# Kernel tuning notes

Measured on AMD Instinct MI355X. Metric: run time of the kernel, lower is better.

Reference implementation:

```python
import jax, jax.numpy as jnp
import numpy as np

N = 50000
NEG_SLOPE = 0.2  # PyG GATConv default leaky_relu slope


def _gat_layer(x, src, dst, W, a_s, a_d, b):
    # x: [N, Fin]; W: [Fin, H*C]; a_s, a_d: [H, C]; b: [C]
    H, C = a_s.shape
    xp = (x @ W).reshape(N, H, C)                      # projected node features per head
    alpha_s = jnp.einsum('nhc,hc->nh', xp, a_s)        # [N, H]
    alpha_d = jnp.einsum('nhc,hc->nh', xp, a_d)        # [N, H]
    e = jax.nn.leaky_relu(alpha_s[src] + alpha_d[dst], NEG_SLOPE)  # [E, H]
    # segment softmax over incoming edges of each dst node
    m = jax.ops.segment_max(e, dst, num_segments=N)
    m = jnp.where(jnp.isfinite(m), m, 0.0)
    p = jnp.exp(e - jax.lax.stop_gradient(m)[dst])
    denom = jax.ops.segment_sum(p, dst, num_segments=N)
    alpha = p / denom[dst]                             # [E, H]
    # scatter-aggregate messages
    out = jax.ops.segment_sum(alpha[:, :, None] * xp[src], dst, num_segments=N)  # [N, H, C]
    return out.mean(axis=1) + b                        # concat=False -> mean over heads


def setup_inputs() -> dict:
    key = jax.random.key(0)
    ks = jax.random.split(key, 16)
    IN, HID, OUT, H = 128, 64, 40, 4
    E = 800000
    x = jax.random.normal(ks[0], (N, IN), dtype=jnp.float32)
    edge_index = jax.random.randint(ks[1], (2, E), 0, N, dtype=jnp.int64)

    def mk(kw, ka, fin, fout):
        s = 1.0 / np.sqrt(fin)
        W = jax.random.normal(kw, (fin, H * fout), dtype=jnp.float32) * s
        a_s = jax.random.normal(ka, (H, fout), dtype=jnp.float32) * 0.1
        a_d = jax.random.normal(jax.random.fold_in(ka, 1), (H, fout), dtype=jnp.float32) * 0.1
        b = jnp.zeros((fout,), dtype=jnp.float32)
        return W, a_s, a_d, b

    W1, as1, ad1, b1 = mk(ks[2], ks[3], IN, HID)
    W2, as2, ad2, b2 = mk(ks[4], ks[5], HID, HID)
    W3, as3, ad3, b3 = mk(ks[6], ks[7], HID, OUT)
    return dict(x=x, edge_index=edge_index,
                W1=W1, as1=as1, ad1=ad1, b1=b1,
                W2=W2, as2=as2, ad2=ad2, b2=b2,
                W3=W3, as3=as3, ad3=ad3, b3=b3)


def reference(x, edge_index, W1, as1, ad1, b1, W2, as2, ad2, b2, W3, as3, ad3, b3):
    # PyG GATConv adds self-loops by default
    loop = jnp.arange(N, dtype=edge_index.dtype)
    src = jnp.concatenate([edge_index[0], loop])
    dst = jnp.concatenate([edge_index[1], loop])
    h = jax.nn.relu(_gat_layer(x, src, dst, W1, as1, ad1, b1))   # dropout is identity in eval
    h = jax.nn.relu(_gat_layer(h, src, dst, W2, as2, ad2, b2))
    h = jax.nn.relu(_gat_layer(h, src, dst, W3, as3, ad3, b3))
    return jax.nn.log_softmax(h, axis=-1)
```

## Files before the change

### kernel.cpp

```cpp
#include <hip/hip_runtime.h>
#include <math.h>

#define NNODES 50000
#define NEG_SLOPE 0.2f

typedef unsigned short ushort8v __attribute__((ext_vector_type(8)));
typedef unsigned short ushort4v __attribute__((ext_vector_type(4)));
typedef short short8v __attribute__((ext_vector_type(8)));
typedef float f32x4 __attribute__((ext_vector_type(4)));
typedef float f32x2 __attribute__((ext_vector_type(2)));

__device__ __forceinline__ unsigned short f2bf(float f){
    unsigned u = __float_as_uint(f);
    u += 0x7fff + ((u >> 16) & 1);
    return (unsigned short)(u >> 16);
}

__device__ __forceinline__ void emit_wa(const float* __restrict__ W, const float* __restrict__ a_s,
                                        const float* __restrict__ a_d, unsigned short* __restrict__ Wt,
                                        int Kin, int C, int id){
    const int n = id / Kin, k = id - n * Kin;
    float v = 0.f;
    if(n < 8){
        const int hh = n & 3;
        const float* av = (n < 4) ? a_s : a_d;
        for(int c = 0; c < C; c++) v += W[(size_t)k * (4 * C) + hh * C + c] * av[hh * C + c];
    }
    Wt[id] = f2bf(v);
}

__device__ __forceinline__ void emit_wc(const float* __restrict__ W, unsigned short* __restrict__ Wt,
                                        int Kin, int C, int id){
    const int c = id / (4 * Kin);
    const int hk = id - c * (4 * Kin);
    const int h = hk / Kin, k = hk - h * Kin;
    const float v = (c < C) ? W[(size_t)k * (4 * C) + h * C + c] * 0.25f : 0.f;
    Wt[id] = f2bf(v);
}

__global__ void initprep_kernel(const unsigned long long* __restrict__ e, int* __restrict__ flag,
                                int* __restrict__ deg, int N,
                                const float* __restrict__ x, unsigned short* __restrict__ xbf, int X4,
                                const float* __restrict__ W1, const float* __restrict__ as1, const float* __restrict__ ad1,
                                const float* __restrict__ W2, const float* __restrict__ as2, const float* __restrict__ ad2,
                                const float* __restrict__ W3, const float* __restrict__ as3, const float* __restrict__ ad3,
                                unsigned short* __restrict__ Wa1, unsigned short* __restrict__ Wa2,
                                unsigned short* __restrict__ Wa3, unsigned short* __restrict__ Wc1,
                                unsigned short* __restrict__ Wc2, unsigned short* __restrict__ Wc3){
    if(blockIdx.x == 0 && threadIdx.x < 64){
        const unsigned long long v = e[threadIdx.x];
        const unsigned long long mask = __ballot(v >= (1ULL << 32));
        if(threadIdx.x == 0) *flag = (mask == 0ULL) ? 1 : 0;
    }
    int id = blockIdx.x * blockDim.x + threadIdx.x;
    if(id < N) deg[id] = 0;
    if(id < X4){
        const float4 v = *(const float4*)&x[(size_t)id * 4];
        ushort4v o;
        o[0] = f2bf(v.x); o[1] = f2bf(v.y); o[2] = f2bf(v.z); o[3] = f2bf(v.w);
        *(ushort4v*)&xbf[(size_t)id * 4] = o;
        return;
    }
    id -= X4;
    if(id < 16 * 128){ emit_wa(W1, as1, ad1, Wa1, 128, 64, id); return; }
    id -= 16 * 128;
    if(id < 16 * 64){ emit_wa(W2, as2, ad2, Wa2, 64, 64, id); return; }
    id -= 16 * 64;
    if(id < 16 * 64){ emit_wa(W3, as3, ad3, Wa3, 64, 40, id); return; }
    id -= 16 * 64;
    if(id < 64 * 512){ emit_wc(W1, Wc1, 128, 64, id); return; }
    id -= 64 * 512;
    if(id < 64 * 256){ emit_wc(W2, Wc2, 64, 64, id); return; }
    id -= 64 * 256;
    if(id < 48 * 256){ emit_wc(W3, Wc3, 64, 40, id); }
}

__global__ void hist_kernel(const void* __restrict__ e, const int* __restrict__ flag,
                            int* __restrict__ deg, int E){
    const int i = blockIdx.x * blockDim.x + threadIdx.x;
    if(i < E){
        const int d = (*flag) ? (int)((const long long*)e)[E + i] : ((const int*)e)[E + i];
        atomicAdd(&deg[d], 1);
    }
}

__global__ __launch_bounds__(512) void scan1_kernel(const int* __restrict__ deg,
                                                    int* __restrict__ excl,
                                                    int* __restrict__ bsum, int n){
    __shared__ int sh[512];
    const int t = threadIdx.x;
    const int gid = blockIdx.x * 512 + t;
    const int v = (gid < n) ? deg[gid] : 0;
    sh[t] = v;
    __syncthreads();
    for(int off = 1; off < 512; off <<= 1){
        const int add = (t >= off) ? sh[t - off] : 0;
        __syncthreads();
        sh[t] += add;
        __syncthreads();
    }
    if(gid < n) excl[gid] = sh[t] - v;
    if(t == 511) bsum[blockIdx.x] = sh[511];
}

__global__ __launch_bounds__(128) void scan2_kernel(int* __restrict__ bsum, int nb){
    __shared__ int sh[128];
    const int t = threadIdx.x;
    const int v = (t < nb) ? bsum[t] : 0;
    sh[t] = v;
    __syncthreads();
    for(int off = 1; off < 128; off <<= 1){
        const int add = (t >= off) ? sh[t - off] : 0;
        __syncthreads();
        sh[t] += add;
        __syncthreads();
    }
    if(t < nb) bsum[t] = sh[t] - v;
}

__global__ void scan3_kernel(const int* __restrict__ excl, const int* __restrict__ bsum,
                             int* __restrict__ row_ptr, int* __restrict__ cursor,
                             int n, int E){
    const int gid = blockIdx.x * blockDim.x + threadIdx.x;
    if(gid < n){
        const int r = excl[gid] + bsum[gid >> 9];
        row_ptr[gid] = r;
        cursor[gid] = r;
    }
    if(gid == 0) row_ptr[n] = E;
}

__global__ void scatter_kernel(const void* __restrict__ e, const int* __restrict__ flag,
                               int* __restrict__ cursor, int* __restrict__ col, int E){
    const int i = blockIdx.x * blockDim.x + threadIdx.x;
    if(i < E){
        int s, d;
        if(*flag){ s = (int)((const long long*)e)[i]; d = (int)((const long long*)e)[E + i]; }
        else     { s = ((const int*)e)[i];            d = ((const int*)e)[E + i]; }
        const int pos = atomicAdd(&cursor[d], 1);
        col[pos] = s;
    }
}

template<int K>
__global__ __launch_bounds__(256) void agemm_kernel(const unsigned short* __restrict__ A,
                                                    const unsigned short* __restrict__ Wa,
                                                    float* __restrict__ ea, float* __restrict__ ed,
                                                    int M){
    const int lane = threadIdx.x & 63;
    const int wave = threadIdx.x >> 6;
    const int quad = lane >> 4;
    const int l16 = lane & 15;
    const int bm = blockIdx.x * 64;
    const int m = min(bm + wave * 16 + l16, M - 1);
    f32x4 acc = {0,0,0,0};
    #pragma unroll
    for(int k0 = 0; k0 < K; k0 += 32){
        const short8v a = *(const short8v*)&A[(size_t)m * K + k0 + quad * 8];
        const short8v b = *(const short8v*)&Wa[(size_t)l16 * K + k0 + quad * 8];
        acc = __builtin_amdgcn_mfma_f32_16x16x32_bf16(a, b, acc, 0, 0, 0);
    }
    if(l16 < 8){
        const int h = l16 & 3;
        float* dst = (l16 < 4) ? ea : ed;
        const int rbase = bm + wave * 16 + quad * 4;
        #pragma unroll
        for(int r = 0; r < 4; r++){
            const int row = rbase + r;
            if(row < M){
                const float v = acc[r];
                *(f32x2*)&dst[(size_t)row * 8 + 2 * h] = (f32x2){__expf(v), __expf(NEG_SLOPE * v)};
            }
        }
    }
}

template<int K>
__global__ __launch_bounds__(256) void gather_kernel(const unsigned short* __restrict__ X,
                                                     const int* __restrict__ row_ptr,
                                                     const int* __restrict__ col,
                                                     const float* __restrict__ ea,
                                                     const float* __restrict__ ed,
                                                     unsigned short* __restrict__ g){
    constexpr int CPL = K / 16;
    constexpr int PAIRS = CPL / 2;
    const int lane = threadIdx.x & 63;
    const int wave = threadIdx.x >> 6;
    const int n = blockIdx.x * 4 + wave;
    const int slot = lane >> 4;
    const int pos = lane & 15;
    const int rs = row_ptr[n], re = row_ptr[n + 1];
    const int T = re - rs + 1;
    const float4 edA = *(const float4*)&ed[(size_t)n * 8];
    const float4 edB = *(const float4*)&ed[(size_t)n * 8 + 4];

    f32x2 acc[4][PAIRS];
    #pragma unroll
    for(int h = 0; h < 4; h++)
        #pragma unroll
        for(int p = 0; p < PAIRS; p++) acc[h][p] = (f32x2){0.f, 0.f};
    float dnm[4] = {0.f, 0.f, 0.f, 0.f};

    auto body = [&](int e){
        const int s = (e < re) ? col[e] : n;
        const float4 eaA = *(const float4*)&ea[(size_t)s * 8];
        const float4 eaB = *(const float4*)&ea[(size_t)s * 8 + 4];
        const float w0 = fmaxf(eaA.x * edA.x, eaA.y * edA.y);
        const float w1 = fmaxf(eaA.z * edA.z, eaA.w * edA.w);
        const float w2 = fmaxf(eaB.x * edB.x, eaB.y * edB.y);
        const float w3 = fmaxf(eaB.z * edB.z, eaB.w * edB.w);
        dnm[0] += w0; dnm[1] += w1; dnm[2] += w2; dnm[3] += w3;
        unsigned u[PAIRS];
        if constexpr(PAIRS == 2){
            const uint2 t2 = *(const uint2*)&X[(size_t)s * K + pos * CPL];
            u[0] = t2.x; u[1] = t2.y;
        } else {
            const uint4 t4 = *(const uint4*)&X[(size_t)s * K + pos * CPL];
            u[0] = t4.x; u[1] = t4.y; u[2] = t4.z; u[3] = t4.w;
        }
        #pragma unroll
        for(int p = 0; p < PAIRS; p++){
            const f32x2 v = {__uint_as_float(u[p] << 16), __uint_as_float(u[p] & 0xffff0000u)};
            acc[0][p] += (f32x2){w0, w0} * v;
            acc[1][p] += (f32x2){w1, w1} * v;
            acc[2][p] += (f32x2){w2, w2} * v;
            acc[3][p] += (f32x2){w3, w3} * v;
        }
    };

    int k = 0;
    for(; k + 8 <= T; k += 8){ body(rs + k + slot); body(rs + k + 4 + slot); }
    for(; k + 4 <= T; k += 4){ body(rs + k + slot); }
    if(k < T && slot < T - k){ body(rs + k + slot); }

    #pragma unroll
    for(int msk = 16; msk < 64; msk <<= 1){
        #pragma unroll
        for(int h = 0; h < 4; h++){
            #pragma unroll
            for(int p = 0; p < PAIRS; p++){
                acc[h][p][0] += __shfl_xor(acc[h][p][0], msk);
                acc[h][p][1] += __shfl_xor(acc[h][p][1], msk);
            }
            dnm[h] += __shfl_xor(dnm[h], msk);
        }
    }
    if(lane < 16){
        #pragma unroll
        for(int h = 0; h < 4; h++){
            const float sc = 1.f / dnm[h];
            if constexpr(PAIRS == 2){
                ushort4v o;
                o[0] = f2bf(acc[h][0][0] * sc); o[1] = f2bf(acc[h][0][1] * sc);
                o[2] = f2bf(acc[h][1][0] * sc); o[3] = f2bf(acc[h][1][1] * sc);
                *(ushort4v*)&g[(size_t)n * (4 * K) + h * K + pos * CPL] = o;
            } else {
                ushort8v o;
                #pragma unroll
                for(int p = 0; p < 4; p++){
                    o[2*p]   = f2bf(acc[h][p][0] * sc);
                    o[2*p+1] = f2bf(acc[h][p][1] * sc);
                }
                *(ushort8v*)&g[(size_t)n * (4 * K) + h * K + pos * CPL] = o;
            }
        }
    }
}

template<int KC, int NC, bool FINAL, bool ALPHA>
__global__ __launch_bounds__(256) void pgemm_kernel(const unsigned short* __restrict__ A,
                                                    const unsigned short* __restrict__ Bt,
                                                    const float* __restrict__ bias,
                                                    void* __restrict__ outv,
                                                    const unsigned short* __restrict__ Wa,
                                                    float* __restrict__ ea,
                                                    float* __restrict__ ed,
                                                    int M){
    constexpr int NT = (NC + 15) / 16;
    __shared__ unsigned short lh[ALPHA ? 4 : 1][16][72];
    const int lane = threadIdx.x & 63;
    const int wave = threadIdx.x >> 6;
    const int quad = lane >> 4;
    const int l16 = lane & 15;
    const int bm = blockIdx.x * 64;
    const int m = min(bm + wave * 16 + l16, M - 1);
    const size_t arow = (size_t)m * KC;

    f32x4 acc[NT];
    #pragma unroll
    for(int t = 0; t < NT; t++) acc[t] = (f32x4){0,0,0,0};

    for(int k0 = 0; k0 < KC; k0 += 32){
        const short8v a = *(const short8v*)&A[arow + k0 + quad * 8];
        #pragma unroll
        for(int t = 0; t < NT; t++){
            const short8v b = *(const short8v*)&Bt[(size_t)(t * 16 + l16) * KC + k0 + quad * 8];
            acc[t] = __builtin_amdgcn_mfma_f32_16x16x32_bf16(a, b, acc[t], 0, 0, 0);
        }
    }
    const int rbase = bm + wave * 16 + quad * 4;
    if(!FINAL){
        unsigned short* out = (unsigned short*)outv;
        #pragma unroll
        for(int t = 0; t < NT; t++){
            const int c = t * 16 + l16;
            #pragma unroll
            for(int r = 0; r < 4; r++){
                const unsigned short hb = f2bf(fmaxf(acc[t][r] + bias[c], 0.f));
                const int row = rbase + r;
                if(row < M) out[(size_t)row * NC + c] = hb;
                if constexpr(ALPHA) lh[wave][quad * 4 + r][c] = hb;
            }
        }
        if constexpr(ALPHA){
            f32x4 a4 = {0, 0, 0, 0};
            #pragma unroll
            for(int k0 = 0; k0 < 64; k0 += 32){
                const short8v a = *(const short8v*)&lh[wave][l16][k0 + quad * 8];
                const short8v b = *(const short8v*)&Wa[(size_t)l16 * 64 + k0 + quad * 8];
                a4 = __builtin_amdgcn_mfma_f32_16x16x32_bf16(a, b, a4, 0, 0, 0);
            }
            if(l16 < 8){
                const int h = l16 & 3;
                float* dst = (l16 < 4) ? ea : ed;
                #pragma unroll
                for(int r = 0; r < 4; r++){
                    const int row = rbase + r;
                    if(row < M){
                        const float v = a4[r];
                        *(f32x2*)&dst[(size_t)row * 8 + 2 * h] = (f32x2){__expf(v), __expf(NEG_SLOPE * v)};
                    }
                }
            }
        }
    } else {
        float* out = (float*)outv;
        float o[NT][4];
        #pragma unroll
        for(int t = 0; t < NT; t++){
            const int c = t * 16 + l16;
            const bool valid = c < 40;
            const float bc = valid ? bias[c] : 0.f;
            #pragma unroll
            for(int r = 0; r < 4; r++)
                o[t][r] = valid ? fmaxf(acc[t][r] + bc, 0.f) : -INFINITY;
        }
        #pragma unroll
        for(int r = 0; r < 4; r++){
            float mx = o[0][r];
            #pragma unroll
            for(int t = 1; t < NT; t++) mx = fmaxf(mx, o[t][r]);
            #pragma unroll
            for(int off = 1; off < 16; off <<= 1) mx = fmaxf(mx, __shfl_xor(mx, off));
            float se = 0.f;
            #pragma unroll
            for(int t = 0; t < NT; t++) se += (o[t][r] > -INFINITY) ? __expf(o[t][r] - mx) : 0.f;
            #pragma unroll
            for(int off = 1; off < 16; off <<= 1) se += __shfl_xor(se, off);
            const float lz = mx + logf(se);
            const int row = rbase + r;
            if(row < M){
                #pragma unroll
                for(int t = 0; t < NT; t++){
                    const int c = t * 16 + l16;
                    if(c < 40) out[(size_t)row * 40 + c] = o[t][r] - lz;
                }
            }
        }
    }
}

extern "C" void kernel_launch(void* const* d_in, const int* in_sizes, int n_in,
                              void* d_out, int out_size, void* d_ws, size_t ws_size,
                              hipStream_t stream){
    const int N = NNODES;
    const int E = in_sizes[1] / 2;

    const float* x   = (const float*)d_in[0];
    const float* W1  = (const float*)d_in[2];
    const float* as1 = (const float*)d_in[3];
    const float* ad1 = (const float*)d_in[4];
    const float* b1  = (const float*)d_in[5];
    const float* W2  = (const float*)d_in[6];
    const float* as2 = (const float*)d_in[7];
    const float* ad2 = (const float*)d_in[8];
    const float* b2  = (const float*)d_in[9];
    const float* W3  = (const float*)d_in[10];
    const float* as3 = (const float*)d_in[11];
    const float* ad3 = (const float*)d_in[12];
    const float* b3  = (const float*)d_in[13];

    char* ws = (char*)d_ws;
    size_t off = 0;
    auto alloc = [&](size_t bytes) -> void* {
        void* p = ws + off;
        off = (off + bytes + 255) & ~(size_t)255;
        return p;
    };
    int*   flag    = (int*)  alloc(4);
    int*   row_ptr = (int*)  alloc((size_t)(N + 1) * 4);
    int*   colv    = (int*)  alloc((size_t)E * 4);
    int*   cursor  = (int*)  alloc((size_t)N * 4);
    int*   deg     = (int*)  alloc((size_t)N * 4);
    int*   excl    = (int*)  alloc((size_t)N * 4);
    int*   bsum    = (int*)  alloc(128 * 4);
    unsigned short* xbf = (unsigned short*)alloc((size_t)N * 128 * 2);
    unsigned short* Wa1 = (unsigned short*)alloc(16 * 128 * 2);
    unsigned short* Wa2 = (unsigned short*)alloc(16 * 64 * 2);
    unsigned short* Wa3 = (unsigned short*)alloc(16 * 64 * 2);
    unsigned short* Wc1 = (unsigned short*)alloc((size_t)64 * 512 * 2);
    unsigned short* Wc2 = (unsigned short*)alloc((size_t)64 * 256 * 2);
    unsigned short* Wc3 = (unsigned short*)alloc((size_t)48 * 256 * 2);
    float* eav     = (float*)alloc((size_t)N * 8 * 4);
    float* edv     = (float*)alloc((size_t)N * 8 * 4);
    unsigned short* g   = (unsigned short*)alloc((size_t)N * 512 * 2);
    unsigned short* h1  = (unsigned short*)alloc((size_t)N * 64 * 2);
    unsigned short* h2  = (unsigned short*)alloc((size_t)N * 64 * 2);
    (void)ws_size;

    const void* eraw = d_in[1];

    const int X4 = N * 128 / 4;
    const int prepTotal = X4 + 16*128 + 16*64 + 16*64 + 64*512 + 64*256 + 48*256;
    initprep_kernel<<<(prepTotal + 255) / 256, 256, 0, stream>>>(
        (const unsigned long long*)eraw, flag, deg, N, x, xbf, X4,
        W1, as1, ad1, W2, as2, ad2, W3, as3, ad3,
        Wa1, Wa2, Wa3, Wc1, Wc2, Wc3);

    hist_kernel<<<(E + 255) / 256, 256, 0, stream>>>(eraw, flag, deg, E);
    const int nbScan = (N + 511) / 512;
    scan1_kernel<<<nbScan, 512, 0, stream>>>(deg, excl, bsum, N);
    scan2_kernel<<<1, 128, 0, stream>>>(bsum, nbScan);
    scan3_kernel<<<(N + 255) / 256, 256, 0, stream>>>(excl, bsum, row_ptr, cursor, N, E);
    scatter_kernel<<<(E + 255) / 256, 256, 0, stream>>>(eraw, flag, cursor, colv, E);

    const int nodeBlocks = N / 4;
    const int mBlocks = (N + 63) / 64;

    agemm_kernel<128><<<mBlocks, 256, 0, stream>>>(xbf, Wa1, eav, edv, N);
    gather_kernel<128><<<nodeBlocks, 256, 0, stream>>>(xbf, row_ptr, colv, eav, edv, g);
    pgemm_kernel<512, 64, false, true><<<mBlocks, 256, 0, stream>>>(g, Wc1, b1, h1, Wa2, eav, edv, N);

    gather_kernel<64><<<nodeBlocks, 256, 0, stream>>>(h1, row_ptr, colv, eav, edv, g);
    pgemm_kernel<256, 64, false, true><<<mBlocks, 256, 0, stream>>>(g, Wc2, b2, h2, Wa3, eav, edv, N);

    gather_kernel<64><<<nodeBlocks, 256, 0, stream>>>(h2, row_ptr, colv, eav, edv, g);
    pgemm_kernel<256, 40, true, false><<<mBlocks, 256, 0, stream>>>(g, Wc3, b3, d_out, nullptr, nullptr, nullptr, N);
}
```

Before: 428.5 us.

## Fuse neighbor gather with projection GEMM via shared memory per 16-node tile

Merges the per-layer gather kernel and the projection GEMM into one kernel. Each 256-thread block aggregates 16 destination nodes (4 per wave) into LDS, then runs MFMA against the head-concatenated weights, writing h or the final log-softmax directly. The per-node attention logits are double-buffered so the next layer's ea/ed can be written while the current ones are being read. This removes the large intermediate g buffer round-trip and three launches. The cost is fewer waves in flight per node during the gather and an extra block-level sync.

Result: faster. 419.3 us (-2.1%).

```diff
diff --git a/kernel.cpp b/kernel.cpp
--- a/kernel.cpp
+++ b/kernel.cpp
@@ -175,158 +175,147 @@
     }
 }
 
-template<int K>
-__global__ __launch_bounds__(256) void gather_kernel(const unsigned short* __restrict__ X,
-                                                     const int* __restrict__ row_ptr,
-                                                     const int* __restrict__ col,
-                                                     const float* __restrict__ ea,
-                                                     const float* __restrict__ ed,
-                                                     unsigned short* __restrict__ g){
-    constexpr int CPL = K / 16;
-    constexpr int PAIRS = CPL / 2;
-    const int lane = threadIdx.x & 63;
-    const int wave = threadIdx.x >> 6;
-    const int n = blockIdx.x * 4 + wave;
-    const int slot = lane >> 4;
-    const int pos = lane & 15;
-    const int rs = row_ptr[n], re = row_ptr[n + 1];
-    const int T = re - rs + 1;
-    const float4 edA = *(const float4*)&ed[(size_t)n * 8];
-    const float4 edB = *(const float4*)&ed[(size_t)n * 8 + 4];
-
-    f32x2 acc[4][PAIRS];
-    #pragma unroll
-    for(int h = 0; h < 4; h++)
-        #pragma unroll
-        for(int p = 0; p < PAIRS; p++) acc[h][p] = (f32x2){0.f, 0.f};
-    float dnm[4] = {0.f, 0.f, 0.f, 0.f};
-
-    auto body = [&](int e){
-        const int s = (e < re) ? col[e] : n;
-        const float4 eaA = *(const float4*)&ea[(size_t)s * 8];
-        const float4 eaB = *(const float4*)&ea[(size_t)s * 8 + 4];
-        const float w0 = fmaxf(eaA.x * edA.x, eaA.y * edA.y);
-        const float w1 = fmaxf(eaA.z * edA.z, eaA.w * edA.w);
-        const float w2 = fmaxf(eaB.x * edB.x, eaB.y * edB.y);
-        const float w3 = fmaxf(eaB.z * edB.z, eaB.w * edB.w);
-        dnm[0] += w0; dnm[1] += w1; dnm[2] += w2; dnm[3] += w3;
-        unsigned u[PAIRS];
-        if constexpr(PAIRS == 2){
-            const uint2 t2 = *(const uint2*)&X[(size_t)s * K + pos * CPL];
-            u[0] = t2.x; u[1] = t2.y;
-        } else {
-            const uint4 t4 = *(const uint4*)&X[(size_t)s * K + pos * CPL];
-            u[0] = t4.x; u[1] = t4.y; u[2] = t4.z; u[3] = t4.w;
-        }
-        #pragma unroll
-        for(int p = 0; p < PAIRS; p++){
-            const f32x2 v = {__uint_as_float(u[p] << 16), __uint_as_float(u[p] & 0xffff0000u)};
-            acc[0][p] += (f32x2){w0, w0} * v;
-            acc[1][p] += (f32x2){w1, w1} * v;
-            acc[2][p] += (f32x2){w2, w2} * v;
-            acc[3][p] += (f32x2){w3, w3} * v;
-        }
-    };
-
-    int k = 0;
-    for(; k + 8 <= T; k += 8){ body(rs + k + slot); body(rs + k + 4 + slot); }
-    for(; k + 4 <= T; k += 4){ body(rs + k + slot); }
-    if(k < T && slot < T - k){ body(rs + k + slot); }
-
-    #pragma unroll
-    for(int msk = 16; msk < 64; msk <<= 1){
-        #pragma unroll
-        for(int h = 0; h < 4; h++){
-            #pragma unroll
-            for(int p = 0; p < PAIRS; p++){
-                acc[h][p][0] += __shfl_xor(acc[h][p][0], msk);
-                acc[h][p][1] += __shfl_xor(acc[h][p][1], msk);
-            }
-            dnm[h] += __shfl_xor(dnm[h], msk);
-        }
-    }
-    if(lane < 16){
-        #pragma unroll
-        for(int h = 0; h < 4; h++){
-            const float sc = 1.f / dnm[h];
-            if constexpr(PAIRS == 2){
-                ushort4v o;
-                o[0] = f2bf(acc[h][0][0] * sc); o[1] = f2bf(acc[h][0][1] * sc);
-                o[2] = f2bf(acc[h][1][0] * sc); o[3] = f2bf(acc[h][1][1] * sc);
-                *(ushort4v*)&g[(size_t)n * (4 * K) + h * K + pos * CPL] = o;
-            } else {
-                ushort8v o;
-                #pragma unroll
-                for(int p = 0; p < 4; p++){
-                    o[2*p]   = f2bf(acc[h][p][0] * sc);
-                    o[2*p+1] = f2bf(acc[h][p][1] * sc);
-                }
-                *(ushort8v*)&g[(size_t)n * (4 * K) + h * K + pos * CPL] = o;
-            }
-        }
-    }
-}
-
-template<int KC, int NC, bool FINAL, bool ALPHA>
-__global__ __launch_bounds__(256) void pgemm_kernel(const unsigned short* __restrict__ A,
+template<int K, int NC, bool FINAL, bool ALPHA>
+__global__ __launch_bounds__(256) void fused_kernel(const unsigned short* __restrict__ X,
+                                                    const int* __restrict__ row_ptr,
+                                                    const int* __restrict__ col,
+                                                    const float* __restrict__ ea,
+                                                    const float* __restrict__ ed,
                                                     const unsigned short* __restrict__ Bt,
                                                     const float* __restrict__ bias,
                                                     void* __restrict__ outv,
                                                     const unsigned short* __restrict__ Wa,
-                                                    float* __restrict__ ea,
-                                                    float* __restrict__ ed,
-                                                    int M){
-    constexpr int NT = (NC + 15) / 16;
-    __shared__ unsigned short lh[ALPHA ? 4 : 1][16][72];
+                                                    float* __restrict__ ea_o,
+                                                    float* __restrict__ ed_o){
+    constexpr int KC = 4 * K;
+    constexpr int CPL = K / 16;
+    constexpr int PAIRS = CPL / 2;
+    constexpr int LSTR = KC + 8;
+    __shared__ unsigned short lg[16][LSTR];
+    __shared__ unsigned short lh[ALPHA ? 16 : 1][72];
+    __shared__ float lo[FINAL ? 16 : 1][48];
+
     const int lane = threadIdx.x & 63;
     const int wave = threadIdx.x >> 6;
-    const int quad = lane >> 4;
-    const int l16 = lane & 15;
-    const int bm = blockIdx.x * 64;
-    const int m = min(bm + wave * 16 + l16, M - 1);
-    const size_t arow = (size_t)m * KC;
-
-    f32x4 acc[NT];
-    #pragma unroll
-    for(int t = 0; t < NT; t++) acc[t] = (f32x4){0,0,0,0};
-
-    for(int k0 = 0; k0 < KC; k0 += 32){
-        const short8v a = *(const short8v*)&A[arow + k0 + quad * 8];
-        #pragma unroll
-        for(int t = 0; t < NT; t++){
-            const short8v b = *(const short8v*)&Bt[(size_t)(t * 16 + l16) * KC + k0 + quad * 8];
-            acc[t] = __builtin_amdgcn_mfma_f32_16x16x32_bf16(a, b, acc[t], 0, 0, 0);
-        }
-    }
-    const int rbase = bm + wave * 16 + quad * 4;
-    if(!FINAL){
+    const int slot = lane >> 4;
+    const int pos  = lane & 15;
+    const int nb   = blockIdx.x * 16;
+
+    #pragma unroll 1
+    for(int i = 0; i < 4; i++){
+        const int row16 = wave * 4 + i;
+        const int n = nb + row16;
+        const int rs = row_ptr[n], re = row_ptr[n + 1];
+        const int T = re - rs + 1;
+        const float4 edA = *(const float4*)&ed[(size_t)n * 8];
+        const float4 edB = *(const float4*)&ed[(size_t)n * 8 + 4];
+
+        f32x2 acc[4][PAIRS];
+        #pragma unroll
+        for(int h = 0; h < 4; h++)
+            #pragma unroll
+            for(int p = 0; p < PAIRS; p++) acc[h][p] = (f32x2){0.f, 0.f};
+        float dnm[4] = {0.f, 0.f, 0.f, 0.f};
+
+        auto body = [&](int e){
+            const int s = (e < re) ? col[e] : n;
+            const float4 eaA = *(const float4*)&ea[(size_t)s * 8];
+            const float4 eaB = *(const float4*)&ea[(size_t)s * 8 + 4];
+            const float w0 = fmaxf(eaA.x * edA.x, eaA.y * edA.y);
+            const float w1 = fmaxf(eaA.z * edA.z, eaA.w * edA.w);
+            const float w2 = fmaxf(eaB.x * edB.x, eaB.y * edB.y);
+            const float w3 = fmaxf(eaB.z * edB.z, eaB.w * edB.w);
+            dnm[0] += w0; dnm[1] += w1; dnm[2] += w2; dnm[3] += w3;
+            unsigned u[PAIRS];
+            if constexpr(PAIRS == 2){
+                const uint2 t2 = *(const uint2*)&X[(size_t)s * K + pos * CPL];
+                u[0] = t2.x; u[1] = t2.y;
+            } else {
+                const uint4 t4 = *(const uint4*)&X[(size_t)s * K + pos * CPL];
+                u[0] = t4.x; u[1] = t4.y; u[2] = t4.z; u[3] = t4.w;
+            }
+            #pragma unroll
+            for(int p = 0; p < PAIRS; p++){
+                const f32x2 v = {__uint_as_float(u[p] << 16), __uint_as_float(u[p] & 0xffff0000u)};
+                acc[0][p] += (f32x2){w0, w0} * v;
+                acc[1][p] += (f32x2){w1, w1} * v;
+                acc[2][p] += (f32x2){w2, w2} * v;
+                acc[3][p] += (f32x2){w3, w3} * v;
+            }
+        };
+
+        int k = 0;
+        for(; k + 8 <= T; k += 8){ body(rs + k + slot); body(rs + k + 4 + slot); }
+        for(; k + 4 <= T; k += 4){ body(rs + k + slot); }
+        if(k < T && slot < T - k){ body(rs + k + slot); }
+
+        #pragma unroll
+        for(int msk = 16; msk < 64; msk <<= 1){
+            #pragma unroll
+            for(int h = 0; h < 4; h++){
+                #pragma unroll
+                for(int p = 0; p < PAIRS; p++){
+                    acc[h][p][0] += __shfl_xor(acc[h][p][0], msk);
+                    acc[h][p][1] += __shfl_xor(acc[h][p][1], msk);
+                }
+                dnm[h] += __shfl_xor(dnm[h], msk);
+            }
+        }
+        if(lane < 16){
+            #pragma unroll
+            for(int h = 0; h < 4; h++){
+                const float sc = 1.f / dnm[h];
+                if constexpr(PAIRS == 2){
+                    ushort4v o;
+                    o[0] = f2bf(acc[h][0][0] * sc); o[1] = f2bf(acc[h][0][1] * sc);
+                    o[2] = f2bf(acc[h][1][0] * sc); o[3] = f2bf(acc[h][1][1] * sc);
+                    *(ushort4v*)&lg[row16][h * K + pos * CPL] = o;
+                } else {
+                    ushort8v o;
+                    #pragma unroll
+                    for(int p = 0; p < 4; p++){
+                        o[2*p]   = f2bf(acc[h][p][0] * sc);
+                        o[2*p+1] = f2bf(acc[h][p][1] * sc);
+                    }
+                    *(ushort8v*)&lg[row16][h * K + pos * CPL] = o;
+                }
+            }
+        }
+    }
+    __syncthreads();
+
+    if constexpr(!FINAL){
+        f32x4 acc4 = {0, 0, 0, 0};
+        const int c = wave * 16 + pos;
+        for(int k0 = 0; k0 < KC; k0 += 32){
+            const short8v a = *(const short8v*)&lg[pos][k0 + slot * 8];
+            const short8v b = *(const short8v*)&Bt[(size_t)c * KC + k0 + slot * 8];
+            acc4 = __builtin_amdgcn_mfma_f32_16x16x32_bf16(a, b, acc4, 0, 0, 0);
+        }
         unsigned short* out = (unsigned short*)outv;
-        #pragma unroll
-        for(int t = 0; t < NT; t++){
-            const int c = t * 16 + l16;
-            #pragma unroll
-            for(int r = 0; r < 4; r++){
-                const unsigned short hb = f2bf(fmaxf(acc[t][r] + bias[c], 0.f));
-                const int row = rbase + r;
-                if(row < M) out[(size_t)row * NC + c] = hb;
-                if constexpr(ALPHA) lh[wave][quad * 4 + r][c] = hb;
-            }
+        const float bc = bias[c];
+        #pragma unroll
+        for(int r = 0; r < 4; r++){
+            const unsigned short hb = f2bf(fmaxf(acc4[r] + bc, 0.f));
+            out[(size_t)(nb + slot * 4 + r) * NC + c] = hb;
+            if constexpr(ALPHA) lh[slot * 4 + r][c] = hb;
         }
         if constexpr(ALPHA){
-            f32x4 a4 = {0, 0, 0, 0};
-            #pragma unroll
-            for(int k0 = 0; k0 < 64; k0 += 32){
-                const short8v a = *(const short8v*)&lh[wave][l16][k0 + quad * 8];
-                const short8v b = *(const short8v*)&Wa[(size_t)l16 * 64 + k0 + quad * 8];
-                a4 = __builtin_amdgcn_mfma_f32_16x16x32_bf16(a, b, a4, 0, 0, 0);
-            }
-            if(l16 < 8){
-                const int h = l16 & 3;
-                float* dst = (l16 < 4) ? ea : ed;
+            __syncthreads();
+            if(wave == 0){
+                f32x4 a4 = {0, 0, 0, 0};
                 #pragma unroll
-                for(int r = 0; r < 4; r++){
-                    const int row = rbase + r;
-                    if(row < M){
+                for(int k0 = 0; k0 < 64; k0 += 32){
+                    const short8v a = *(const short8v*)&lh[pos][k0 + slot * 8];
+                    const short8v b = *(const short8v*)&Wa[(size_t)pos * 64 + k0 + slot * 8];
+                    a4 = __builtin_amdgcn_mfma_f32_16x16x32_bf16(a, b, a4, 0, 0, 0);
+                }
+                if(pos < 8){
+                    const int h = pos & 3;
+                    float* dst = (pos < 4) ? ea_o : ed_o;
+                    #pragma unroll
+                    for(int r = 0; r < 4; r++){
+                        const int row = nb + slot * 4 + r;
                         const float v = a4[r];
                         *(f32x2*)&dst[(size_t)row * 8 + 2 * h] = (f32x2){__expf(v), __expf(NEG_SLOPE * v)};
                     }
@@ -334,39 +323,38 @@
             }
         }
     } else {
-        float* out = (float*)outv;
-        float o[NT][4];
-        #pragma unroll
-        for(int t = 0; t < NT; t++){
-            const int c = t * 16 + l16;
+        if(wave < 3){
+            f32x4 acc4 = {0, 0, 0, 0};
+            const int c = wave * 16 + pos;
+            for(int k0 = 0; k0 < KC; k0 += 32){
+                const short8v a = *(const short8v*)&lg[pos][k0 + slot * 8];
+                const short8v b = *(const short8v*)&Bt[(size_t)c * KC + k0 + slot * 8];
+                acc4 = __builtin_amdgcn_mfma_f32_16x16x32_bf16(a, b, acc4, 0, 0, 0);
+            }
             const bool valid = c < 40;
             const float bc = valid ? bias[c] : 0.f;
             #pragma unroll
             for(int r = 0; r < 4; r++)
-                o[t][r] = valid ? fmaxf(acc[t][r] + bc, 0.f) : -INFINITY;
-        }
-        #pragma unroll
-        for(int r = 0; r < 4; r++){
-            float mx = o[0][r];
-            #pragma unroll
-            for(int t = 1; t < NT; t++) mx = fmaxf(mx, o[t][r]);
-            #pragma unroll
-            for(int off = 1; off < 16; off <<= 1) mx = fmaxf(mx, __shfl_xor(mx, off));
-            float se = 0.f;
-            #pragma unroll
-            for(int t = 0; t < NT; t++) se += (o[t][r] > -INFINITY) ? __expf(o[t][r] - mx) : 0.f;
-            #pragma unroll
-            for(int off = 1; off < 16; off <<= 1) se += __shfl_xor(se, off);
-            const float lz = mx + logf(se);
-            const int row = rbase + r;
-            if(row < M){
-                #pragma unroll
-                for(int t = 0; t < NT; t++){
-                    const int c = t * 16 + l16;
-                    if(c < 40) out[(size_t)row * 40 + c] = o[t][r] - lz;
-                }
-            }
-        }
+                lo[slot * 4 + r][c] = valid ? fmaxf(acc4[r] + bc, 0.f) : -INFINITY;
+        }
+        __syncthreads();
+        const int r  = threadIdx.x >> 4;
+        const int cc = threadIdx.x & 15;
+        const float o0 = lo[r][cc];
+        const float o1 = lo[r][cc + 16];
+        const float o2 = lo[r][cc + 32];
+        float mx = fmaxf(fmaxf(o0, o1), o2);
+        #pragma unroll
+        for(int off = 1; off < 16; off <<= 1) mx = fmaxf(mx, __shfl_xor(mx, off));
+        float se = __expf(o0 - mx) + __expf(o1 - mx) + ((o2 > -INFINITY) ? __expf(o2 - mx) : 0.f);
+        #pragma unroll
+        for(int off = 1; off < 16; off <<= 1) se += __shfl_xor(se, off);
+        const float lz = mx + logf(se);
+        float* out = (float*)outv;
+        const size_t rb = (size_t)(nb + r) * 40;
+        out[rb + cc] = o0 - lz;
+        out[rb + cc + 16] = o1 - lz;
+        if(cc < 8) out[rb + cc + 32] = o2 - lz;
     }
 }
 
@@ -411,9 +399,10 @@
     unsigned short* Wc1 = (unsigned short*)alloc((size_t)64 * 512 * 2);
     unsigned short* Wc2 = (unsigned short*)alloc((size_t)64 * 256 * 2);
     unsigned short* Wc3 = (unsigned short*)alloc((size_t)48 * 256 * 2);
-    float* eav     = (float*)alloc((size_t)N * 8 * 4);
-    float* edv     = (float*)alloc((size_t)N * 8 * 4);
-    unsigned short* g   = (unsigned short*)alloc((size_t)N * 512 * 2);
+    float* eav0 = (float*)alloc((size_t)N * 8 * 4);
+    float* edv0 = (float*)alloc((size_t)N * 8 * 4);
+    float* eav1 = (float*)alloc((size_t)N * 8 * 4);
+    float* edv1 = (float*)alloc((size_t)N * 8 * 4);
     unsigned short* h1  = (unsigned short*)alloc((size_t)N * 64 * 2);
     unsigned short* h2  = (unsigned short*)alloc((size_t)N * 64 * 2);
     (void)ws_size;
@@ -434,16 +423,17 @@
     scan3_kernel<<<(N + 255) / 256, 256, 0, stream>>>(excl, bsum, row_ptr, cursor, N, E);
     scatter_kernel<<<(E + 255) / 256, 256, 0, stream>>>(eraw, flag, cursor, colv, E);
 
-    const int nodeBlocks = N / 4;
     const int mBlocks = (N + 63) / 64;
-
-    agemm_kernel<128><<<mBlocks, 256, 0, stream>>>(xbf, Wa1, eav, edv, N);
-    gather_kernel<128><<<nodeBlocks, 256, 0, stream>>>(xbf, row_ptr, colv, eav, edv, g);
-    pgemm_kernel<512, 64, false, true><<<mBlocks, 256, 0, stream>>>(g, Wc1, b1, h1, Wa2, eav, edv, N);
-
-    gather_kernel<64><<<nodeBlocks, 256, 0, stream>>>(h1, row_ptr, colv, eav, edv, g);
-    pgemm_kernel<256, 64, false, true><<<mBlocks, 256, 0, stream>>>(g, Wc2, b2, h2, Wa3, eav, edv, N);
-
-    gather_kernel<64><<<nodeBlocks, 256, 0, stream>>>(h2, row_ptr, colv, eav, edv, g);
-    pgemm_kernel<256, 40, true, false><<<mBlocks, 256, 0, stream>>>(g, Wc3, b3, d_out, nullptr, nullptr, nullptr, N);
-}
+    const int fBlocks = N / 16;
+
+    agemm_kernel<128><<<mBlocks, 256, 0, stream>>>(xbf, Wa1, eav0, edv0, N);
+
+    fused_kernel<128, 64, false, true><<<fBlocks, 256, 0, stream>>>(
+        xbf, row_ptr, colv, eav0, edv0, Wc1, b1, h1, Wa2, eav1, edv1);
+
+    fused_kernel<64, 64, false, true><<<fBlocks, 256, 0, stream>>>(
+        h1, row_ptr, colv, eav1, edv1, Wc2, b2, h2, Wa3, eav0, edv0);
+
+    fused_kernel<64, 40, true, false><<<fBlocks, 256, 0, stream>>>(
+        h2, row_ptr, colv, eav0, edv0, Wc3, b3, d_out, nullptr, nullptr, nullptr);
+}
```

## Compute edge attention weights once per lane and stage them in LDS for gather

Applied to the files above, without the earlier changes.

Restructures the neighbor gather so each lane computes the softmax weight for one edge and writes the source index and per-head weights to shared memory. The whole wave then loops over staged edges, each lane loading a two-feature slice of the source row. This removes redundant per-lane recomputation and duplicate loads of attention logits. In exchange, feature loads are narrower per lane, edges are processed serially per wave, and LDS traffic is added.

Measured after the change: 420.1 us. About the same (-2.0%).

```diff
diff --git a/kernel.cpp b/kernel.cpp
--- a/kernel.cpp
+++ b/kernel.cpp
@@ -176,93 +176,98 @@
 }
 
 template<int K>
-__global__ __launch_bounds__(256) void gather_kernel(const unsigned short* __restrict__ X,
-                                                     const int* __restrict__ row_ptr,
-                                                     const int* __restrict__ col,
-                                                     const float* __restrict__ ea,
-                                                     const float* __restrict__ ed,
-                                                     unsigned short* __restrict__ g){
-    constexpr int CPL = K / 16;
-    constexpr int PAIRS = CPL / 2;
+__global__ __launch_bounds__(256) void gatherg_kernel(const unsigned short* __restrict__ X,
+                                                      const int* __restrict__ row_ptr,
+                                                      const int* __restrict__ col,
+                                                      const float* __restrict__ ea,
+                                                      const float* __restrict__ ed,
+                                                      unsigned short* __restrict__ g){
+    __shared__ int   ls[4][64];
+    __shared__ float lw[4][64][4];
     const int lane = threadIdx.x & 63;
     const int wave = threadIdx.x >> 6;
-    const int n = blockIdx.x * 4 + wave;
-    const int slot = lane >> 4;
-    const int pos = lane & 15;
+    const int n    = blockIdx.x * 4 + wave;
     const int rs = row_ptr[n], re = row_ptr[n + 1];
     const int T = re - rs + 1;
     const float4 edA = *(const float4*)&ed[(size_t)n * 8];
     const float4 edB = *(const float4*)&ed[(size_t)n * 8 + 4];
 
-    f32x2 acc[4][PAIRS];
+    f32x2 acc[4];
     #pragma unroll
-    for(int h = 0; h < 4; h++)
-        #pragma unroll
-        for(int p = 0; p < PAIRS; p++) acc[h][p] = (f32x2){0.f, 0.f};
-    float dnm[4] = {0.f, 0.f, 0.f, 0.f};
-
-    auto body = [&](int e){
-        const int s = (e < re) ? col[e] : n;
-        const float4 eaA = *(const float4*)&ea[(size_t)s * 8];
-        const float4 eaB = *(const float4*)&ea[(size_t)s * 8 + 4];
-        const float w0 = fmaxf(eaA.x * edA.x, eaA.y * edA.y);
-        const float w1 = fmaxf(eaA.z * edA.z, eaA.w * edA.w);
-        const float w2 = fmaxf(eaB.x * edB.x, eaB.y * edB.y);
-        const float w3 = fmaxf(eaB.z * edB.z, eaB.w * edB.w);
-        dnm[0] += w0; dnm[1] += w1; dnm[2] += w2; dnm[3] += w3;
-        unsigned u[PAIRS];
-        if constexpr(PAIRS == 2){
-            const uint2 t2 = *(const uint2*)&X[(size_t)s * K + pos * CPL];
-            u[0] = t2.x; u[1] = t2.y;
+    for(int h = 0; h < 4; h++) acc[h] = (f32x2){0.f, 0.f};
+    float d0 = 0.f, d1 = 0.f, d2 = 0.f, d3 = 0.f;
+
+    const int c2 = (K == 128) ? (lane * 2) : ((lane & 31) * 2);
+    const int eo = lane >> 5;
+
+    for(int base = 0; base < T; base += 64){
+        const int ecnt = min(T - base, 64);
+        if(lane < ecnt){
+            const int e = rs + base + lane;
+            const int s = (e < re) ? col[e] : n;
+            const float4 eaA = *(const float4*)&ea[(size_t)s * 8];
+            const float4 eaB = *(const float4*)&ea[(size_t)s * 8 + 4];
+            const float w0 = fmaxf(eaA.x * edA.x, eaA.y * edA.y);
+            const float w1 = fmaxf(eaA.z * edA.z, eaA.w * edA.w);
+            const float w2 = fmaxf(eaB.x * edB.x, eaB.y * edB.y);
+            const float w3 = fmaxf(eaB.z * edB.z, eaB.w * edB.w);
+            d0 += w0; d1 += w1; d2 += w2; d3 += w3;
+            ls[wave][lane] = s;
+            *(f32x4*)&lw[wave][lane][0] = (f32x4){w0, w1, w2, w3};
+        }
+        if constexpr(K == 128){
+            auto body = [&](int e){
+                const int s = ls[wave][e];
+                const f32x4 w4 = *(const f32x4*)&lw[wave][e][0];
+                const unsigned u = *(const unsigned*)&X[(size_t)s * K + c2];
+                const f32x2 v = {__uint_as_float(u << 16), __uint_as_float(u & 0xffff0000u)};
+                acc[0] += (f32x2){w4[0], w4[0]} * v;
+                acc[1] += (f32x2){w4[1], w4[1]} * v;
+                acc[2] += (f32x2){w4[2], w4[2]} * v;
+                acc[3] += (f32x2){w4[3], w4[3]} * v;
+            };
+            int e = 0;
+            for(; e + 4 <= ecnt; e += 4){ body(e); body(e + 1); body(e + 2); body(e + 3); }
+            for(; e < ecnt; e++) body(e);
         } else {
-            const uint4 t4 = *(const uint4*)&X[(size_t)s * K + pos * CPL];
-            u[0] = t4.x; u[1] = t4.y; u[2] = t4.z; u[3] = t4.w;
-        }
-        #pragma unroll
-        for(int p = 0; p < PAIRS; p++){
-            const f32x2 v = {__uint_as_float(u[p] << 16), __uint_as_float(u[p] & 0xffff0000u)};
-            acc[0][p] += (f32x2){w0, w0} * v;
-            acc[1][p] += (f32x2){w1, w1} * v;
-            acc[2][p] += (f32x2){w2, w2} * v;
-            acc[3][p] += (f32x2){w3, w3} * v;
-        }
-    };
-
-    int k = 0;
-    for(; k + 8 <= T; k += 8){ body(rs + k + slot); body(rs + k + 4 + slot); }
-    for(; k + 4 <= T; k += 4){ body(rs + k + slot); }
-    if(k < T && slot < T - k){ body(rs + k + slot); }
+            auto body = [&](int p){
+                const int e = p + eo;
+                if(e < ecnt){
+                    const int s = ls[wave][e];
+                    const f32x4 w4 = *(const f32x4*)&lw[wave][e][0];
+                    const unsigned u = *(const unsigned*)&X[(size_t)s * K + c2];
+                    const f32x2 v = {__uint_as_float(u << 16), __uint_as_float(u & 0xffff0000u)};
+                    acc[0] += (f32x2){w4[0], w4[0]} * v;
+                    acc[1] += (f32x2){w4[1], w4[1]} * v;
+                    acc[2] += (f32x2){w4[2], w4[2]} * v;
+                    acc[3] += (f32x2){w4[3], w4[3]} * v;
+                }
+            };
+            int p = 0;
+            for(; p + 8 <= ecnt; p += 8){ body(p); body(p + 2); body(p + 4); body(p + 6); }
+            for(; p < ecnt; p += 2) body(p);
+        }
+    }
 
     #pragma unroll
-    for(int msk = 16; msk < 64; msk <<= 1){
+    for(int msk = 1; msk < 64; msk <<= 1){
+        d0 += __shfl_xor(d0, msk); d1 += __shfl_xor(d1, msk);
+        d2 += __shfl_xor(d2, msk); d3 += __shfl_xor(d3, msk);
+    }
+    if constexpr(K == 64){
         #pragma unroll
         for(int h = 0; h < 4; h++){
-            #pragma unroll
-            for(int p = 0; p < PAIRS; p++){
-                acc[h][p][0] += __shfl_xor(acc[h][p][0], msk);
-                acc[h][p][1] += __shfl_xor(acc[h][p][1], msk);
-            }
-            dnm[h] += __shfl_xor(dnm[h], msk);
-        }
-    }
-    if(lane < 16){
+            acc[h][0] += __shfl_xor(acc[h][0], 32);
+            acc[h][1] += __shfl_xor(acc[h][1], 32);
+        }
+    }
+    const float invs[4] = {1.f / d0, 1.f / d1, 1.f / d2, 1.f / d3};
+    if(K == 128 || lane < 32){
         #pragma unroll
         for(int h = 0; h < 4; h++){
-            const float sc = 1.f / dnm[h];
-            if constexpr(PAIRS == 2){
-                ushort4v o;
-                o[0] = f2bf(acc[h][0][0] * sc); o[1] = f2bf(acc[h][0][1] * sc);
-                o[2] = f2bf(acc[h][1][0] * sc); o[3] = f2bf(acc[h][1][1] * sc);
-                *(ushort4v*)&g[(size_t)n * (4 * K) + h * K + pos * CPL] = o;
-            } else {
-                ushort8v o;
-                #pragma unroll
-                for(int p = 0; p < 4; p++){
-                    o[2*p]   = f2bf(acc[h][p][0] * sc);
-                    o[2*p+1] = f2bf(acc[h][p][1] * sc);
-                }
-                *(ushort8v*)&g[(size_t)n * (4 * K) + h * K + pos * CPL] = o;
-            }
+            const unsigned lo = f2bf(acc[h][0] * invs[h]);
+            const unsigned hi = f2bf(acc[h][1] * invs[h]);
+            *(unsigned*)&g[(size_t)n * (4 * K) + h * K + c2] = lo | (hi << 16);
         }
     }
 }
@@ -438,12 +443,12 @@
     const int mBlocks = (N + 63) / 64;
 
     agemm_kernel<128><<<mBlocks, 256, 0, stream>>>(xbf, Wa1, eav, edv, N);
-    gather_kernel<128><<<nodeBlocks, 256, 0, stream>>>(xbf, row_ptr, colv, eav, edv, g);
+    gatherg_kernel<128><<<nodeBlocks, 256, 0, stream>>>(xbf, row_ptr, colv, eav, edv, g);
     pgemm_kernel<512, 64, false, true><<<mBlocks, 256, 0, stream>>>(g, Wc1, b1, h1, Wa2, eav, edv, N);
 
-    gather_kernel<64><<<nodeBlocks, 256, 0, stream>>>(h1, row_ptr, colv, eav, edv, g);
+    gatherg_kernel<64><<<nodeBlocks, 256, 0, stream>>>(h1, row_ptr, colv, eav, edv, g);
     pgemm_kernel<256, 64, false, true><<<mBlocks, 256, 0, stream>>>(g, Wc2, b2, h2, Wa3, eav, edv, N);
 
-    gather_kernel<64><<<nodeBlocks, 256, 0, stream>>>(h2, row_ptr, colv, eav, edv, g);
+    gatherg_kernel<64><<<nodeBlocks, 256, 0, stream>>>(h2, row_ptr, colv, eav, edv, g);
     pgemm_kernel<256, 40, true, false><<<mBlocks, 256, 0, stream>>>(g, Wc3, b3, d_out, nullptr, nullptr, nullptr, N);
 }
```
